# Performance work log

Hardware: AMD Instinct MI355X
Metric: run time of the kernel (lower is better)

Reference implementation:

```python
import jax, jax.numpy as jnp
import numpy as np

N = 50000

def gcn_conv(h, W, b, src, dst, n):
    # h: [N, Fin] -> linear transform then normalized scatter-add aggregation
    h = h @ W  # [N, Fout]
    # add self-loops (PyG GCNConv default)
    loop = jnp.arange(n, dtype=src.dtype)
    s = jnp.concatenate([src, loop])
    d = jnp.concatenate([dst, loop])
    # symmetric normalization: deg^{-1/2}[s] * deg^{-1/2}[d], deg over target index
    deg = jax.ops.segment_sum(jnp.ones_like(d, dtype=h.dtype), d, num_segments=n)
    dinv = jnp.where(deg > 0, jax.lax.rsqrt(deg), 0.0)
    norm = dinv[s] * dinv[d]  # [E+N]
    msg = h[s] * norm[:, None]  # gather + scale
    out = jax.ops.segment_sum(msg, d, num_segments=n)  # scatter-add
    return out + b


def setup_inputs() -> dict:
    key = jax.random.key(0)
    k1, k2, k3, k4, k5, k6 = jax.random.split(key, 6)
    Fin, Fh, Fout = 512, 256, 64
    E = 800000
    x = jax.random.normal(k1, (N, Fin), dtype=jnp.float32)
    edge_index = jax.random.randint(k2, (2, E), 0, N, dtype=jnp.int64)
    # Glorot-style init matching nn Parameter scale
    W1 = jax.random.normal(k3, (Fin, Fh), dtype=jnp.float32) * (1.0 / np.sqrt(Fin))
    b1 = jnp.zeros((Fh,), dtype=jnp.float32)
    W2 = jax.random.normal(k4, (Fh, Fout), dtype=jnp.float32) * (1.0 / np.sqrt(Fh))
    b2 = jnp.zeros((Fout,), dtype=jnp.float32)
    return {"x": x, "edge_index": edge_index, "W1": W1, "b1": b1, "W2": W2, "b2": b2}


def reference(x, edge_index, W1, b1, W2, b2):
    src, dst = edge_index[0], edge_index[1]
    h1 = jax.nn.relu(gcn_conv(x, W1, b1, src, dst, N))
    # dropout is identity in eval mode
    h2 = gcn_conv(h1, W2, b2, src, dst, N)
    return jax.nn.log_softmax(h2, axis=1)
```

## Files before the change

kernel.cpp:

```cpp
#include <hip/hip_runtime.h>
#include <hip/hip_bf16.h>

typedef __attribute__((ext_vector_type(8))) short short8;
typedef __attribute__((ext_vector_type(4))) float f32x4;

#define NNODES 50000

#define FENCE_BAR() asm volatile("s_waitcnt lgkmcnt(0)\n\ts_barrier" ::: "memory")

__device__ __forceinline__ float b2f(unsigned short s) {
  union { unsigned int u; float f; } c; c.u = ((unsigned int)s) << 16;
  return c.f;
}
__device__ __forceinline__ unsigned short f2b(float f) {
  return __bfloat16_as_ushort(__float2bfloat16(f));
}
__device__ __forceinline__ unsigned int pkcvt(float a, float b) {
  return (unsigned int)f2b(a) | ((unsigned int)f2b(b) << 16);
}

__global__ __launch_bounds__(256) void k_deg(const int* __restrict__ ei, int* __restrict__ deg, int E,
                                             const float* __restrict__ W1, const float* __restrict__ W2,
                                             unsigned short* __restrict__ w1t, unsigned short* __restrict__ w2t) {
  int idx = blockIdx.x * 256 + threadIdx.x;
  if (idx < E) atomicAdd(&deg[ei[E + idx]], 1);
  if (idx < 256 * 512) { int nn = idx >> 9, kk = idx & 511; w1t[idx] = f2b(W1[kk * 256 + nn]); }
  int i2 = idx - 256 * 512;
  if (i2 >= 0 && i2 < 64 * 256) { int nn = i2 >> 8, kk = i2 & 255; w2t[i2] = f2b(W2[kk * 64 + nn]); }
}

__global__ __launch_bounds__(256) void k_scanA(const int* __restrict__ deg, int* __restrict__ excl,
                                               int* __restrict__ blksum, float* __restrict__ dinv, int n) {
  const int i = blockIdx.x * 256 + threadIdx.x;
  const int lane = threadIdx.x & 63, wid = threadIdx.x >> 6;
  const int v = (i < n) ? deg[i] : 0;
  int x = v;
#pragma unroll
  for (int o = 1; o < 64; o <<= 1) {
    int y = __shfl_up(x, o, 64);
    if (lane >= o) x += y;
  }
  __shared__ int wsum[4];
  if (lane == 63) wsum[wid] = x;
  __syncthreads();
  int woff = 0;
  for (int w = 0; w < wid; ++w) woff += wsum[w];
  const int incl = x + woff;
  if (i < n) {
    excl[i] = incl - v;
    dinv[i] = rsqrtf((float)v + 1.0f);
  }
  if (threadIdx.x == 255) blksum[blockIdx.x] = incl;
}

__global__ __launch_bounds__(256) void k_scanC(const int* __restrict__ excl, const int* __restrict__ blksum,
                                               int* __restrict__ rowptr, int* __restrict__ cursor, int n, int E) {
  const int t = threadIdx.x;
  int partial = 0;
  for (int j = t; j < (int)blockIdx.x; j += 256) partial += blksum[j];
#pragma unroll
  for (int o = 32; o > 0; o >>= 1) partial += __shfl_xor(partial, o, 64);
  __shared__ int ws[4];
  if ((t & 63) == 0) ws[t >> 6] = partial;
  __syncthreads();
  const int off = ws[0] + ws[1] + ws[2] + ws[3];
  const int i = blockIdx.x * 256 + t;
  if (i < n) {
    int r = excl[i] + off;
    rowptr[i] = r;
    cursor[i] = r;
  }
  if (i == 0) rowptr[n] = E;
}

__global__ __launch_bounds__(256) void k_fill(const int* __restrict__ ei, int* __restrict__ cursor,
                                              int* __restrict__ csr, int E) {
  int e = blockIdx.x * 256 + threadIdx.x;
  if (e < E) {
    int pos = atomicAdd(&cursor[ei[E + e]], 1);
    csr[pos] = ei[e];
  }
}

__global__ __launch_bounds__(256) void k_gemm1(const float* __restrict__ x,
    const unsigned short* __restrict__ w1t, const float* __restrict__ dinv,
    unsigned short* __restrict__ hs1b) {
  const int M = NNODES, K = 512, N = 256;
  const int NRB = (NNODES + 63) / 64;
  const int bid = blockIdx.x;
  const int rowblk = (bid >> 5) * 8 + (bid & 7);
  const int colblk = (bid >> 3) & 3;
  if (rowblk >= NRB) return;

  __shared__ unsigned short As[2][64][36];
  __shared__ unsigned short Bs[2][64][36];
  const int tid = threadIdx.x;
  const int brow = rowblk * 64, bcol = colblk * 64;
  const int wid = tid >> 6, lane = tid & 63;
  const int wr = wid >> 1, wc = wid & 1;
  const int lr = lane & 15, lk = lane >> 4;
  const int r = tid >> 2, q = tid & 3;

  f32x4 acc[2][2] = {};

  int arow = brow + r; if (arow >= M) arow = M - 1;
  const float* aptr = x + (size_t)arow * K + q * 8;
  const unsigned short* bptr = w1t + (size_t)(bcol + r) * K + q * 8;

  float4 a0, a1;
  uint4 bv;

#define G1_LOAD(KOFF) do { \
    a0 = *(const float4*)(aptr + (KOFF)); \
    a1 = *(const float4*)(aptr + (KOFF) + 4); \
    bv = *(const uint4*)(bptr + (KOFF)); \
  } while (0)

#define G1_STAGE(BUF) do { \
    uint4 pa_; \
    pa_.x = pkcvt(a0.x, a0.y); pa_.y = pkcvt(a0.z, a0.w); \
    pa_.z = pkcvt(a1.x, a1.y); pa_.w = pkcvt(a1.z, a1.w); \
    *(uint4*)&As[BUF][r][q * 8] = pa_; \
    *(uint4*)&Bs[BUF][r][q * 8] = bv; \
  } while (0)

  G1_LOAD(0);
  G1_STAGE(0);
  G1_LOAD(32);
  __syncthreads();

  for (int s = 0; s < 16; ++s) {
    const int cur = s & 1;
    short8 af[2], bf[2];
#pragma unroll
    for (int m = 0; m < 2; ++m) af[m] = *(const short8*)&As[cur][wr * 32 + m * 16 + lr][lk * 8];
#pragma unroll
    for (int n = 0; n < 2; ++n) bf[n] = *(const short8*)&Bs[cur][wc * 32 + n * 16 + lr][lk * 8];
    if (s < 15) G1_STAGE(cur ^ 1);
    if (s < 14) G1_LOAD((s + 2) * 32);
#pragma unroll
    for (int m = 0; m < 2; ++m)
#pragma unroll
      for (int n = 0; n < 2; ++n)
        acc[m][n] = __builtin_amdgcn_mfma_f32_16x16x32_bf16(af[m], bf[n], acc[m][n], 0, 0, 0);
    FENCE_BAR();
  }

#pragma unroll
  for (int m = 0; m < 2; ++m) {
#pragma unroll
    for (int n = 0; n < 2; ++n) {
      const int col = bcol + wc * 32 + n * 16 + lr;
#pragma unroll
      for (int j = 0; j < 4; ++j) {
        const int row = brow + wr * 32 + m * 16 + lk * 4 + j;
        if (row < M) hs1b[(size_t)row * N + col] = f2b(acc[m][n][j] * dinv[row]);
      }
    }
  }
#undef G1_LOAD
#undef G1_STAGE
}

__global__ __launch_bounds__(256) void k_agg1g(const int* __restrict__ rowptr,
    const int* __restrict__ csr, const unsigned short* __restrict__ hs1b,
    const float* __restrict__ dinv, const float* __restrict__ b1,
    const unsigned short* __restrict__ w2t, unsigned short* __restrict__ hs2b) {
  const int M = NNODES;
  __shared__ unsigned short h1t[16][264];
  const int tid = threadIdx.x;
  const int w = tid >> 6, lane = tid & 63;
  const int lr = lane & 15, lk = lane >> 4;
  const int brow = blockIdx.x * 16;

  const float4 bb = *(const float4*)(b1 + lane * 4);

  for (int i = 0; i < 4; ++i) {
    const int ldsrow = w * 4 + i;
    const int d = brow + ldsrow;
    f32x4 acc = {0.f, 0.f, 0.f, 0.f};
    if (d < M) {
      const int a = rowptr[d], bnd = rowptr[d + 1];
      ushort4 sv = *(const ushort4*)(hs1b + (size_t)d * 256 + lane * 4);
      acc[0] = b2f(sv.x); acc[1] = b2f(sv.y); acc[2] = b2f(sv.z); acc[3] = b2f(sv.w);
      int e = a;
      for (; e + 8 <= bnd; e += 8) {
        int s[8];
#pragma unroll
        for (int j = 0; j < 8; ++j) s[j] = csr[e + j];
        ushort4 v[8];
#pragma unroll
        for (int j = 0; j < 8; ++j) v[j] = *(const ushort4*)(hs1b + (size_t)s[j] * 256 + lane * 4);
#pragma unroll
        for (int j = 0; j < 8; ++j) {
          acc[0] += b2f(v[j].x); acc[1] += b2f(v[j].y);
          acc[2] += b2f(v[j].z); acc[3] += b2f(v[j].w);
        }
      }
      for (; e + 2 <= bnd; e += 2) {
        int s0 = csr[e], s1 = csr[e + 1];
        ushort4 v0 = *(const ushort4*)(hs1b + (size_t)s0 * 256 + lane * 4);
        ushort4 v1 = *(const ushort4*)(hs1b + (size_t)s1 * 256 + lane * 4);
        acc[0] += b2f(v0.x) + b2f(v1.x); acc[1] += b2f(v0.y) + b2f(v1.y);
        acc[2] += b2f(v0.z) + b2f(v1.z); acc[3] += b2f(v0.w) + b2f(v1.w);
      }
      for (; e < bnd; ++e) {
        int s0 = csr[e];
        ushort4 v0 = *(const ushort4*)(hs1b + (size_t)s0 * 256 + lane * 4);
        acc[0] += b2f(v0.x); acc[1] += b2f(v0.y); acc[2] += b2f(v0.z); acc[3] += b2f(v0.w);
      }
      const float di = dinv[d];
      acc[0] = fmaxf(0.f, acc[0] * di + bb.x);
      acc[1] = fmaxf(0.f, acc[1] * di + bb.y);
      acc[2] = fmaxf(0.f, acc[2] * di + bb.z);
      acc[3] = fmaxf(0.f, acc[3] * di + bb.w);
    }
    uint2 pk;
    pk.x = pkcvt(acc[0], acc[1]);
    pk.y = pkcvt(acc[2], acc[3]);
    *(uint2*)&h1t[ldsrow][lane * 4] = pk;
  }

  __syncthreads();

  f32x4 acc2 = {};
#pragma unroll
  for (int s = 0; s < 8; ++s) {
    short8 af = *(const short8*)&h1t[lr][s * 32 + lk * 8];
    short8 bfv = *(const short8*)(w2t + (size_t)(w * 16 + lr) * 256 + s * 32 + lk * 8);
    acc2 = __builtin_amdgcn_mfma_f32_16x16x32_bf16(af, bfv, acc2, 0, 0, 0);
  }

  {
    const int col = w * 16 + lr;
#pragma unroll
    for (int j = 0; j < 4; ++j) {
      const int row = brow + lk * 4 + j;
      if (row < M) hs2b[(size_t)row * 64 + col] = f2b(acc2[j] * dinv[row]);
    }
  }
}

__global__ __launch_bounds__(256) void k_agg2f(const int* __restrict__ rowptr,
    const int* __restrict__ csr, const unsigned short* __restrict__ hs2b,
    const float* __restrict__ dinv, const float* __restrict__ b2,
    float* __restrict__ out) {
  const int d = blockIdx.x * 4 + (threadIdx.x >> 6);
  if (d >= NNODES) return;
  const int lane = threadIdx.x & 63;
  const int a = rowptr[d], bnd = rowptr[d + 1];

  float acc = b2f(hs2b[(size_t)d * 64 + lane]);

  int i = a;
  for (; i + 8 <= bnd; i += 8) {
    int s[8];
#pragma unroll
    for (int j = 0; j < 8; ++j) s[j] = csr[i + j];
    unsigned short v[8];
#pragma unroll
    for (int j = 0; j < 8; ++j) v[j] = hs2b[(size_t)s[j] * 64 + lane];
#pragma unroll
    for (int j = 0; j < 8; ++j) acc += b2f(v[j]);
  }
  for (; i < bnd; ++i) acc += b2f(hs2b[(size_t)csr[i] * 64 + lane]);

  float v = acc * dinv[d] + b2[lane];
  float m = v;
#pragma unroll
  for (int o = 32; o > 0; o >>= 1) m = fmaxf(m, __shfl_xor(m, o, 64));
  float ex = expf(v - m);
  float s = ex;
#pragma unroll
  for (int o = 32; o > 0; o >>= 1) s += __shfl_xor(s, o, 64);
  out[(size_t)d * 64 + lane] = v - m - logf(s);
}

extern "C" void kernel_launch(void* const* d_in, const int* in_sizes, int n_in,
                              void* d_out, int out_size, void* d_ws, size_t ws_size,
                              hipStream_t stream) {
  const float* x  = (const float*)d_in[0];
  const int*   ei = (const int*)d_in[1];
  const float* W1 = (const float*)d_in[2];
  const float* b1 = (const float*)d_in[3];
  const float* W2 = (const float*)d_in[4];
  const float* b2 = (const float*)d_in[5];
  float* out = (float*)d_out;
  const int E = in_sizes[1] / 2;
  const int n = NNODES;
  const int nblk = (n + 255) / 256;

  char* ws = (char*)d_ws;
  size_t off = 0;
  auto alloc = [&](size_t bytes) { char* p = ws + off; off = (off + bytes + 255) & ~(size_t)255; return p; };
  int*            deg    = (int*)alloc((size_t)n * 4);
  float*          dinv   = (float*)alloc((size_t)n * 4);
  int*            excl   = (int*)alloc((size_t)n * 4);
  int*            blksum = (int*)alloc((size_t)nblk * 4);
  int*            rowptr = (int*)alloc((size_t)(n + 1) * 4);
  int*            cursor = (int*)alloc((size_t)n * 4);
  int*            csr    = (int*)alloc((size_t)E * 4);
  unsigned short* w1t    = (unsigned short*)alloc(256 * 512 * 2);
  unsigned short* w2t    = (unsigned short*)alloc(64 * 256 * 2);
  unsigned short* hs1b   = (unsigned short*)alloc((size_t)n * 256 * 2);
  unsigned short* hs2b   = (unsigned short*)alloc((size_t)n * 64 * 2);
  (void)ws_size; (void)n_in; (void)out_size;

  hipMemsetAsync(deg, 0, (size_t)n * 4, stream);
  k_deg<<<(E + 255) / 256, 256, 0, stream>>>(ei, deg, E, W1, W2, w1t, w2t);
  k_scanA<<<nblk, 256, 0, stream>>>(deg, excl, blksum, dinv, n);
  k_scanC<<<nblk, 256, 0, stream>>>(excl, blksum, rowptr, cursor, n, E);
  k_fill<<<(E + 255) / 256, 256, 0, stream>>>(ei, cursor, csr, E);
  k_gemm1<<<98 * 32, 256, 0, stream>>>(x, w1t, dinv, hs1b);
  k_agg1g<<<(n + 15) / 16, 256, 0, stream>>>(rowptr, csr, hs1b, dinv, b1, w2t, hs2b);
  k_agg2f<<<(n + 3) / 4, 256, 0, stream>>>(rowptr, csr, hs2b, dinv, b2, out);
}
```

Baseline: 252.4 us.

## Pre-convert x to bf16 and use direct global-to-LDS loads in GEMM1

Moves the fp32-to-bf16 conversion of x into the prologue kernel, writing a bf16 copy to workspace. GEMM1 then stages A and B tiles with global_load_lds straight into unpadded LDS, and the row tile grows to 128 so each wave issues 8 MFMAs per k-step. The aim is to cut register staging and conversion work inside the GEMM loop. The cost is an extra full pass that reads x and writes the bf16 copy, and the unpadded LDS layout may cause bank conflicts on fragment reads.

Measured after the change: 256.6 us. About the same (+1.7%).

```diff
diff --git a/kernel.cpp b/kernel.cpp
--- a/kernel.cpp
+++ b/kernel.cpp
@@ -6,7 +6,7 @@
 
 #define NNODES 50000
 
-#define FENCE_BAR() asm volatile("s_waitcnt lgkmcnt(0)\n\ts_barrier" ::: "memory")
+#define VM_BAR() asm volatile("s_waitcnt vmcnt(0)\n\ts_barrier" ::: "memory")
 
 __device__ __forceinline__ float b2f(unsigned short s) {
   union { unsigned int u; float f; } c; c.u = ((unsigned int)s) << 16;
@@ -19,14 +19,28 @@
   return (unsigned int)f2b(a) | ((unsigned int)f2b(b) << 16);
 }
 
+__device__ __forceinline__ void gl_lds16(const void* g, void* l) {
+  __builtin_amdgcn_global_load_lds((const __attribute__((address_space(1))) unsigned int*)g,
+                                   (__attribute__((address_space(3))) unsigned int*)l, 16, 0, 0);
+}
+
 __global__ __launch_bounds__(256) void k_deg(const int* __restrict__ ei, int* __restrict__ deg, int E,
                                              const float* __restrict__ W1, const float* __restrict__ W2,
-                                             unsigned short* __restrict__ w1t, unsigned short* __restrict__ w2t) {
+                                             unsigned short* __restrict__ w1t, unsigned short* __restrict__ w2t,
+                                             const float* __restrict__ x, unsigned short* __restrict__ xb) {
   int idx = blockIdx.x * 256 + threadIdx.x;
   if (idx < E) atomicAdd(&deg[ei[E + idx]], 1);
   if (idx < 256 * 512) { int nn = idx >> 9, kk = idx & 511; w1t[idx] = f2b(W1[kk * 256 + nn]); }
   int i2 = idx - 256 * 512;
   if (i2 >= 0 && i2 < 64 * 256) { int nn = i2 >> 8, kk = i2 & 255; w2t[i2] = f2b(W2[kk * 64 + nn]); }
+  if (idx < (NNODES * 512) / 8) {
+    const float4 v0 = *(const float4*)(x + (size_t)idx * 8);
+    const float4 v1 = *(const float4*)(x + (size_t)idx * 8 + 4);
+    uint4 p;
+    p.x = pkcvt(v0.x, v0.y); p.y = pkcvt(v0.z, v0.w);
+    p.z = pkcvt(v1.x, v1.y); p.w = pkcvt(v1.z, v1.w);
+    *(uint4*)(xb + (size_t)idx * 8) = p;
+  }
 }
 
 __global__ __launch_bounds__(256) void k_scanA(const int* __restrict__ deg, int* __restrict__ excl,
@@ -82,84 +96,74 @@
   }
 }
 
-__global__ __launch_bounds__(256) void k_gemm1(const float* __restrict__ x,
+__global__ __launch_bounds__(256) void k_gemm1(const unsigned short* __restrict__ xb,
     const unsigned short* __restrict__ w1t, const float* __restrict__ dinv,
     unsigned short* __restrict__ hs1b) {
   const int M = NNODES, K = 512, N = 256;
-  const int NRB = (NNODES + 63) / 64;
+  const int NRB = (NNODES + 127) / 128;
   const int bid = blockIdx.x;
   const int rowblk = (bid >> 5) * 8 + (bid & 7);
   const int colblk = (bid >> 3) & 3;
   if (rowblk >= NRB) return;
 
-  __shared__ unsigned short As[2][64][36];
-  __shared__ unsigned short Bs[2][64][36];
+  __shared__ unsigned short Ab[2][128][32];
+  __shared__ unsigned short Bb[2][64][32];
+
   const int tid = threadIdx.x;
-  const int brow = rowblk * 64, bcol = colblk * 64;
-  const int wid = tid >> 6, lane = tid & 63;
-  const int wr = wid >> 1, wc = wid & 1;
+  const int w = tid >> 6, lane = tid & 63;
+  const int sub = lane >> 2, c = lane & 3;
+  const int brow = rowblk * 128, bcol = colblk * 64;
+  const int wr = w >> 1, wc = w & 1;
   const int lr = lane & 15, lk = lane >> 4;
-  const int r = tid >> 2, q = tid & 3;
-
-  f32x4 acc[2][2] = {};
-
-  int arow = brow + r; if (arow >= M) arow = M - 1;
-  const float* aptr = x + (size_t)arow * K + q * 8;
-  const unsigned short* bptr = w1t + (size_t)(bcol + r) * K + q * 8;
-
-  float4 a0, a1;
-  uint4 bv;
-
-#define G1_LOAD(KOFF) do { \
-    a0 = *(const float4*)(aptr + (KOFF)); \
-    a1 = *(const float4*)(aptr + (KOFF) + 4); \
-    bv = *(const uint4*)(bptr + (KOFF)); \
+
+  int gr0 = brow + w * 16 + sub;      if (gr0 >= M) gr0 = M - 1;
+  int gr1 = brow + 64 + w * 16 + sub; if (gr1 >= M) gr1 = M - 1;
+  const int grB = bcol + w * 16 + sub;
+
+  const unsigned short* a0p = xb + (size_t)gr0 * K + c * 8;
+  const unsigned short* a1p = xb + (size_t)gr1 * K + c * 8;
+  const unsigned short* bp  = w1t + (size_t)grB * K + c * 8;
+
+  f32x4 acc[4][2] = {};
+
+#define G1_STAGE(BUF, KT) do { \
+    gl_lds16(a0p + (KT), &Ab[BUF][w * 16][0]); \
+    gl_lds16(a1p + (KT), &Ab[BUF][64 + w * 16][0]); \
+    gl_lds16(bp  + (KT), &Bb[BUF][w * 16][0]); \
   } while (0)
 
-#define G1_STAGE(BUF) do { \
-    uint4 pa_; \
-    pa_.x = pkcvt(a0.x, a0.y); pa_.y = pkcvt(a0.z, a0.w); \
-    pa_.z = pkcvt(a1.x, a1.y); pa_.w = pkcvt(a1.z, a1.w); \
-    *(uint4*)&As[BUF][r][q * 8] = pa_; \
-    *(uint4*)&Bs[BUF][r][q * 8] = bv; \
-  } while (0)
-
-  G1_LOAD(0);
-  G1_STAGE(0);
-  G1_LOAD(32);
-  __syncthreads();
+  G1_STAGE(0, 0);
+  VM_BAR();
 
   for (int s = 0; s < 16; ++s) {
     const int cur = s & 1;
-    short8 af[2], bf[2];
-#pragma unroll
-    for (int m = 0; m < 2; ++m) af[m] = *(const short8*)&As[cur][wr * 32 + m * 16 + lr][lk * 8];
-#pragma unroll
-    for (int n = 0; n < 2; ++n) bf[n] = *(const short8*)&Bs[cur][wc * 32 + n * 16 + lr][lk * 8];
-    if (s < 15) G1_STAGE(cur ^ 1);
-    if (s < 14) G1_LOAD((s + 2) * 32);
-#pragma unroll
-    for (int m = 0; m < 2; ++m)
+    if (s < 15) G1_STAGE(cur ^ 1, (s + 1) * 32);
+    short8 af[4], bf[2];
+#pragma unroll
+    for (int m = 0; m < 4; ++m) af[m] = *(const short8*)&Ab[cur][wr * 64 + m * 16 + lr][lk * 8];
+#pragma unroll
+    for (int n = 0; n < 2; ++n) bf[n] = *(const short8*)&Bb[cur][wc * 32 + n * 16 + lr][lk * 8];
+#pragma unroll
+    for (int m = 0; m < 4; ++m)
 #pragma unroll
       for (int n = 0; n < 2; ++n)
         acc[m][n] = __builtin_amdgcn_mfma_f32_16x16x32_bf16(af[m], bf[n], acc[m][n], 0, 0, 0);
-    FENCE_BAR();
-  }
-
-#pragma unroll
-  for (int m = 0; m < 2; ++m) {
+    VM_BAR();
+  }
+#undef G1_STAGE
+
+#pragma unroll
+  for (int m = 0; m < 4; ++m) {
 #pragma unroll
     for (int n = 0; n < 2; ++n) {
       const int col = bcol + wc * 32 + n * 16 + lr;
 #pragma unroll
       for (int j = 0; j < 4; ++j) {
-        const int row = brow + wr * 32 + m * 16 + lk * 4 + j;
+        const int row = brow + wr * 64 + m * 16 + lk * 4 + j;
         if (row < M) hs1b[(size_t)row * N + col] = f2b(acc[m][n][j] * dinv[row]);
       }
     }
   }
-#undef G1_LOAD
-#undef G1_STAGE
 }
 
 __global__ __launch_bounds__(256) void k_agg1g(const int* __restrict__ rowptr,
@@ -304,14 +308,15 @@
   unsigned short* w2t    = (unsigned short*)alloc(64 * 256 * 2);
   unsigned short* hs1b   = (unsigned short*)alloc((size_t)n * 256 * 2);
   unsigned short* hs2b   = (unsigned short*)alloc((size_t)n * 64 * 2);
+  unsigned short* xb     = (unsigned short*)alloc((size_t)n * 512 * 2);
   (void)ws_size; (void)n_in; (void)out_size;
 
   hipMemsetAsync(deg, 0, (size_t)n * 4, stream);
-  k_deg<<<(E + 255) / 256, 256, 0, stream>>>(ei, deg, E, W1, W2, w1t, w2t);
+  k_deg<<<(NNODES * 512 / 8 + 255) / 256, 256, 0, stream>>>(ei, deg, E, W1, W2, w1t, w2t, x, xb);
   k_scanA<<<nblk, 256, 0, stream>>>(deg, excl, blksum, dinv, n);
   k_scanC<<<nblk, 256, 0, stream>>>(excl, blksum, rowptr, cursor, n, E);
   k_fill<<<(E + 255) / 256, 256, 0, stream>>>(ei, cursor, csr, E);
-  k_gemm1<<<98 * 32, 256, 0, stream>>>(x, w1t, dinv, hs1b);
+  k_gemm1<<<49 * 32, 256, 0, stream>>>(xb, w1t, dinv, hs1b);
   k_agg1g<<<(n + 15) / 16, 256, 0, stream>>>(rowptr, csr, hs1b, dinv, b1, w2t, hs2b);
   k_agg2f<<<(n + 3) / 4, 256, 0, stream>>>(rowptr, csr, hs2b, dinv, b2, out);
 }
```
